# Performance work log

Hardware: AMD Instinct MI355X
Metric: run time of the kernel (lower is better)

The kernel has to match this reference:

```python
import jax, jax.numpy as jnp
import numpy as np

B, T, C = 4, 2048, 1024
H = 16
D = C // H  # head_dim = 64


def setup_inputs() -> dict:
    key = jax.random.key(0)
    ks = jax.random.split(key, 9)
    s = 1.0 / np.sqrt(C)
    return {
        "x": jax.random.normal(ks[0], (B, T, C), dtype=jnp.float32),
        "wq": jax.random.uniform(ks[1], (C, C), jnp.float32, -s, s),
        "bq": jax.random.uniform(ks[2], (C,), jnp.float32, -s, s),
        "wk": jax.random.uniform(ks[3], (C, C), jnp.float32, -s, s),
        "bk": jax.random.uniform(ks[4], (C,), jnp.float32, -s, s),
        "wv": jax.random.uniform(ks[5], (C, C), jnp.float32, -s, s),
        "bv": jax.random.uniform(ks[6], (C,), jnp.float32, -s, s),
        "wo": jax.random.uniform(ks[7], (C, C), jnp.float32, -s, s),
        "bo": jax.random.uniform(ks[8], (C,), jnp.float32, -s, s),
    }


def reference(x, wq, bq, wk, bk, wv, bv, wo, bo):
    # Linear layers (torch convention: y = x @ W.T + b)
    q = x @ wq.T + bq  # [B,T,C]
    k = x @ wk.T + bk
    v = x @ wv.T + bv
    # split heads -> [B,H,T,D]
    q = q.reshape(B, T, H, D).transpose(0, 2, 1, 3)
    k = k.reshape(B, T, H, D).transpose(0, 2, 1, 3)
    v = v.reshape(B, T, H, D).transpose(0, 2, 1, 3)
    scores = jnp.einsum('bhqd,bhkd->bhqk', q, k) / jnp.sqrt(jnp.float32(D))
    causal = jnp.tril(jnp.ones((T, T), dtype=bool))  # position i attends to j<=i
    scores = jnp.where(causal, scores, -jnp.inf)
    attn = jax.nn.softmax(scores, axis=-1)
    # dropout p=0.0 (eval / identity)
    out = jnp.einsum('bhqk,bhkd->bhqd', attn, v)  # [B,H,T,D]
    out = out.transpose(0, 2, 1, 3).reshape(B, T, C)
    return out @ wo.T + bo
```

## Files before the change

### kernel.cpp

```cpp
#include <hip/hip_runtime.h>
#include <stdint.h>

#define B_DIM 4
#define T_DIM 2048
#define C_DIM 1024
#define H_DIM 16
#define D_DIM 64
#define M_DIM (B_DIM * T_DIM)
#define QK_SCALE 0.18033688011112042f

typedef float f32x4 __attribute__((ext_vector_type(4)));
typedef float f32x16 __attribute__((ext_vector_type(16)));
typedef short bf16x8 __attribute__((ext_vector_type(8)));
typedef unsigned short u16;
typedef u16 u16x8 __attribute__((ext_vector_type(8)));

static __device__ __forceinline__ u16 f2b(float f) {
  uint32_t r;
  asm("v_cvt_pk_bf16_f32 %0, %1, %1" : "=v"(r) : "v"(f));
  return (u16)r;
}
static __device__ __forceinline__ uint32_t f2b2(float a, float b) {
  uint32_t r;
  asm("v_cvt_pk_bf16_f32 %0, %1, %2" : "=v"(r) : "v"(a), "v"(b));
  return r;
}

static __device__ __forceinline__ void gl_lds16(const u16* g, u16* l) {
  __builtin_amdgcn_global_load_lds(
      (const __attribute__((address_space(1))) void*)g,
      (__attribute__((address_space(3))) void*)l, 16, 0, 0);
}

__global__ void k_cvt(const float* __restrict__ src, u16* __restrict__ dst, int n4) {
  int i = blockIdx.x * blockDim.x + threadIdx.x;
  if (i < n4) {
    float4 v = ((const float4*)src)[i];
    uint2 o;
    o.x = f2b2(v.x, v.y);
    o.y = f2b2(v.z, v.w);
    ((uint2*)dst)[i] = o;
  }
}

__global__ void k_cvtw(const float* __restrict__ s0, const float* __restrict__ s1,
                       const float* __restrict__ s2, const float* __restrict__ s3,
                       u16* __restrict__ d0, u16* __restrict__ d1,
                       u16* __restrict__ d2, u16* __restrict__ d3) {
  int i = blockIdx.x * blockDim.x + threadIdx.x;
  int seg = i >> 18;
  int j = i & ((1 << 18) - 1);
  const float* s = seg == 0 ? s0 : seg == 1 ? s1 : seg == 2 ? s2 : s3;
  u16* d = seg == 0 ? d0 : seg == 1 ? d1 : seg == 2 ? d2 : d3;
  float4 v = ((const float4*)s)[j];
  uint2 o;
  o.x = f2b2(v.x, v.y);
  o.y = f2b2(v.z, v.w);
  ((uint2*)d)[j] = o;
}

__global__ __launch_bounds__(256) void k_gemm_qkv(
    const u16* __restrict__ A,
    const u16* __restrict__ w0, const u16* __restrict__ w1, const u16* __restrict__ w2,
    const float* __restrict__ b0, const float* __restrict__ b1, const float* __restrict__ b2,
    u16* __restrict__ Qo, u16* __restrict__ Ko, u16* __restrict__ Vo) {
  __shared__ u16 As[128 * 32];
  __shared__ u16 Bs[128 * 32];
  const int tid = threadIdx.x;
  const int l = tid & 63;
  const int w = tid >> 6;
  const int wr = w >> 1, wc = w & 1;
  const int seg = blockIdx.x >> 3;
  const int brow = blockIdx.y * 128, bcol = (blockIdx.x & 7) * 128;
  const int lrow = l & 15, lk = l >> 4;
  const int K = C_DIM;

  const u16* Bw = seg == 0 ? w0 : seg == 1 ? w1 : w2;
  const float* bias = seg == 0 ? b0 : seg == 1 ? b1 : b2;
  u16* Out = seg == 0 ? Qo : seg == 1 ? Ko : Vo;
  const float scale = seg == 0 ? QK_SCALE : 1.f;

  f32x4 acc[4][4];
  for (int m = 0; m < 4; ++m)
    for (int n = 0; n < 4; ++n)
      acc[m][n] = (f32x4){0.f, 0.f, 0.f, 0.f};

  for (int kt = 0; kt < K; kt += 32) {
    __syncthreads();
    {
      int slot = tid;
      int r0 = slot >> 2, c0 = slot & 3;
      gl_lds16(A + (size_t)(brow + r0) * K + kt + c0 * 8, As + slot * 8);
      gl_lds16(Bw + (size_t)(bcol + r0) * K + kt + c0 * 8, Bs + slot * 8);
      int slot2 = slot + 256;
      int r1 = slot2 >> 2, c1 = slot2 & 3;
      gl_lds16(A + (size_t)(brow + r1) * K + kt + c1 * 8, As + slot2 * 8);
      gl_lds16(Bw + (size_t)(bcol + r1) * K + kt + c1 * 8, Bs + slot2 * 8);
    }
    asm volatile("s_waitcnt vmcnt(0)" ::: "memory");
    __syncthreads();

    bf16x8 af[4], bfr[4];
#pragma unroll
    for (int m = 0; m < 4; ++m)
      af[m] = *(const bf16x8*)(As + (wr * 64 + m * 16 + lrow) * 32 + lk * 8);
#pragma unroll
    for (int n = 0; n < 4; ++n)
      bfr[n] = *(const bf16x8*)(Bs + (wc * 64 + n * 16 + lrow) * 32 + lk * 8);
#pragma unroll
    for (int m = 0; m < 4; ++m) {
#pragma unroll
      for (int n = 0; n < 4; ++n)
        acc[m][n] = __builtin_amdgcn_mfma_f32_16x16x32_bf16(af[m], bfr[n], acc[m][n], 0, 0, 0);
    }
  }

#pragma unroll
  for (int m = 0; m < 4; ++m) {
    int rg0 = brow + wr * 64 + m * 16 + lk * 4;
#pragma unroll
    for (int n = 0; n < 4; ++n) {
      int cg = bcol + wc * 64 + n * 16 + lrow;
      float bv = bias[cg];
#pragma unroll
      for (int i = 0; i < 4; ++i) {
        int rg = rg0 + i;
        float val = (acc[m][n][i] + bv) * scale;
        int bb = rg >> 11, tt = rg & (T_DIM - 1);
        int hh = cg >> 6, dd = cg & 63;
        Out[(((size_t)bb * H_DIM + hh) * T_DIM + tt) * D_DIM + dd] = f2b(val);
      }
    }
  }
}

__global__ __launch_bounds__(256) void k_gemm_proj(
    const u16* __restrict__ A, const u16* __restrict__ Bw,
    const float* __restrict__ bias, float* __restrict__ Cout) {
  __shared__ u16 As[128 * 32];
  __shared__ u16 Bs[128 * 32];
  const int tid = threadIdx.x;
  const int l = tid & 63;
  const int w = tid >> 6;
  const int wr = w >> 1, wc = w & 1;
  const int brow = blockIdx.y * 128, bcol = blockIdx.x * 128;
  const int lrow = l & 15, lk = l >> 4;
  const int K = C_DIM, N = C_DIM;

  f32x4 acc[4][4];
  for (int m = 0; m < 4; ++m)
    for (int n = 0; n < 4; ++n)
      acc[m][n] = (f32x4){0.f, 0.f, 0.f, 0.f};

  for (int kt = 0; kt < K; kt += 32) {
    __syncthreads();
    {
      int slot = tid;
      int r0 = slot >> 2, c0 = slot & 3;
      gl_lds16(A + (size_t)(brow + r0) * K + kt + c0 * 8, As + slot * 8);
      gl_lds16(Bw + (size_t)(bcol + r0) * K + kt + c0 * 8, Bs + slot * 8);
      int slot2 = slot + 256;
      int r1 = slot2 >> 2, c1 = slot2 & 3;
      gl_lds16(A + (size_t)(brow + r1) * K + kt + c1 * 8, As + slot2 * 8);
      gl_lds16(Bw + (size_t)(bcol + r1) * K + kt + c1 * 8, Bs + slot2 * 8);
    }
    asm volatile("s_waitcnt vmcnt(0)" ::: "memory");
    __syncthreads();

    bf16x8 af[4], bfr[4];
#pragma unroll
    for (int m = 0; m < 4; ++m)
      af[m] = *(const bf16x8*)(As + (wr * 64 + m * 16 + lrow) * 32 + lk * 8);
#pragma unroll
    for (int n = 0; n < 4; ++n)
      bfr[n] = *(const bf16x8*)(Bs + (wc * 64 + n * 16 + lrow) * 32 + lk * 8);
#pragma unroll
    for (int m = 0; m < 4; ++m) {
#pragma unroll
      for (int n = 0; n < 4; ++n)
        acc[m][n] = __builtin_amdgcn_mfma_f32_16x16x32_bf16(af[m], bfr[n], acc[m][n], 0, 0, 0);
    }
  }

#pragma unroll
  for (int m = 0; m < 4; ++m) {
    int rg0 = brow + wr * 64 + m * 16 + lk * 4;
#pragma unroll
    for (int n = 0; n < 4; ++n) {
      int cg = bcol + wc * 64 + n * 16 + lrow;
      float bv = bias[cg];
#pragma unroll
      for (int i = 0; i < 4; ++i)
        Cout[(size_t)(rg0 + i) * N + cg] = acc[m][n][i] + bv;
    }
  }
}

__global__ __launch_bounds__(256) void k_transpose(
    const u16* __restrict__ V, u16* __restrict__ Vt) {
  __shared__ u16 tile[64][65];
  const int tid = threadIdx.x;
  const int bh = blockIdx.y;
  const int t0 = blockIdx.x * 64;
  const size_t ibase = (size_t)bh * T_DIM * D_DIM + (size_t)t0 * D_DIM;
  const size_t obase = (size_t)bh * D_DIM * T_DIM + t0;

#pragma unroll
  for (int it = 0; it < 2; ++it) {
    int row = (tid >> 3) + it * 32;
    int blk = tid & 7;
    u16x8 v = *(const u16x8*)(V + ibase + (size_t)row * D_DIM + blk * 8);
#pragma unroll
    for (int j = 0; j < 8; ++j) tile[row][blk * 8 + j] = v[j];
  }
  __syncthreads();
#pragma unroll
  for (int it = 0; it < 2; ++it) {
    int d = (tid >> 3) + it * 32;
    int blk = tid & 7;
    u16x8 v;
#pragma unroll
    for (int j = 0; j < 8; ++j) v[j] = tile[blk * 8 + j][d];
    *(u16x8*)(Vt + obase + (size_t)d * T_DIM + blk * 8) = v;
  }
}

__global__ __launch_bounds__(256) void k_attn(
    const u16* __restrict__ Q, const u16* __restrict__ Kg,
    const u16* __restrict__ Vt, u16* __restrict__ O) {
  __shared__ u16 Ks[2][64 * 64];
  __shared__ u16 Vs[2][64 * 64];

  const int tid = threadIdx.x;
  const int l = tid & 63;
  const int w = tid >> 6;
  const int bh = blockIdx.x;
  const int qb = 15 - blockIdx.y;
  const int q0 = qb * 128;
  const int ql = l & 31;
  const int hi = l >> 5;
  const int r0 = q0 + w * 32;
  const int qg = r0 + ql;

  const size_t qkbase = (size_t)bh * T_DIM * D_DIM;
  const size_t vtbase = (size_t)bh * D_DIM * T_DIM;

  const int sr0 = tid >> 3, sc = tid & 7;
  const int sr1 = (tid + 256) >> 3;
  const int kcol0 = (sc ^ (sr0 & 7)) * 8;
  const int kcol1 = (sc ^ (sr1 & 7)) * 8;

#define STAGE(buf, kt)                                                                   \
  {                                                                                      \
    gl_lds16(Kg + qkbase + (size_t)((kt) * 64 + sr0) * D_DIM + kcol0, Ks[buf] + tid * 8);\
    gl_lds16(Vt + vtbase + (size_t)sr0 * T_DIM + (kt) * 64 + kcol0, Vs[buf] + tid * 8);  \
    gl_lds16(Kg + qkbase + (size_t)((kt) * 64 + sr1) * D_DIM + kcol1,                    \
             Ks[buf] + (tid + 256) * 8);                                                 \
    gl_lds16(Vt + vtbase + (size_t)sr1 * T_DIM + (kt) * 64 + kcol1,                      \
             Vs[buf] + (tid + 256) * 8);                                                 \
  }

  bf16x8 qf[4];
#pragma unroll
  for (int kk = 0; kk < 4; ++kk)
    qf[kk] = *(const bf16x8*)(Q + qkbase + (size_t)qg * D_DIM + kk * 16 + hi * 8);

  f32x16 oacc[2];
#pragma unroll
  for (int dt = 0; dt < 2; ++dt)
#pragma unroll
    for (int r = 0; r < 16; ++r) oacc[dt][r] = 0.f;
  float m_run = -1e30f, l_run = 0.f;

  const int tdiag = r0 >> 6;
  const int nkt = (q0 >> 6) + 2;

  STAGE(0, 0);

  for (int kt = 0; kt < nkt; ++kt) {
    const int cur = kt & 1;
    if (kt + 1 < nkt) {
      STAGE(cur ^ 1, kt + 1);
      asm volatile("s_waitcnt vmcnt(4)" ::: "memory");
    } else {
      asm volatile("s_waitcnt vmcnt(0)" ::: "memory");
    }
    __syncthreads();

    if (kt <= tdiag) {
      f32x16 s[2];
#pragma unroll
      for (int a = 0; a < 2; ++a)
#pragma unroll
        for (int r = 0; r < 16; ++r) s[a][r] = 0.f;

#pragma unroll
      for (int kk = 0; kk < 4; ++kk) {
#pragma unroll
        for (int a = 0; a < 2; ++a) {
          int row = a * 32 + ql;
          int blk = (kk * 2 + hi) ^ (row & 7);
          bf16x8 kf = *(const bf16x8*)(Ks[cur] + row * 64 + blk * 8);
          s[a] = __builtin_amdgcn_mfma_f32_32x32x16_bf16(kf, qf[kk], s[a], 0, 0, 0);
        }
      }

      if (kt == tdiag) {
#pragma unroll
        for (int a = 0; a < 2; ++a) {
#pragma unroll
          for (int r = 0; r < 16; ++r) {
            int kv = kt * 64 + a * 32 + (r & 3) + 8 * (r >> 2) + 4 * hi;
            if (kv > qg) s[a][r] = -1e30f;
          }
        }
      }

      float t[16];
#pragma unroll
      for (int r = 0; r < 16; ++r) t[r] = fmaxf(s[0][r], s[1][r]);
#pragma unroll
      for (int r = 0; r < 8; ++r) t[r] = fmaxf(t[r], t[r + 8]);
#pragma unroll
      for (int r = 0; r < 4; ++r) t[r] = fmaxf(t[r], t[r + 4]);
      float pm = fmaxf(fmaxf(t[0], t[1]), fmaxf(t[2], t[3]));
      pm = fmaxf(pm, __shfl_xor(pm, 32, 64));

      if (__any(pm > m_run + 8.f)) {
        float mn = fmaxf(m_run, pm);
        float sc = exp2f(m_run - mn);
        m_run = mn;
        l_run *= sc;
#pragma unroll
        for (int dt = 0; dt < 2; ++dt)
#pragma unroll
          for (int r = 0; r < 16; ++r) oacc[dt][r] *= sc;
      }

      float rs0 = 0.f, rs1 = 0.f, rs2 = 0.f, rs3 = 0.f;
#pragma unroll
      for (int a = 0; a < 2; ++a) {
#pragma unroll
        for (int r = 0; r < 16; ++r) {
          float p = exp2f(s[a][r] - m_run);
          s[a][r] = p;
          if ((r & 3) == 0) rs0 += p;
          else if ((r & 3) == 1) rs1 += p;
          else if ((r & 3) == 2) rs2 += p;
          else rs3 += p;
        }
      }
      float rs = (rs0 + rs1) + (rs2 + rs3);
      rs += __shfl_xor(rs, 32, 64);
      l_run += rs;

#pragma unroll
      for (int kk = 0; kk < 4; ++kk) {
        const int a = kk >> 1;
        const int base = (kk & 1) * 8;
        union { uint32_t wd[4]; bf16x8 v; } pf;
#pragma unroll
        for (int i = 0; i < 2; ++i) {
          uint32_t Aw = f2b2(s[a][base + 2 * i], s[a][base + 2 * i + 1]);
          uint32_t Bw = f2b2(s[a][base + 4 + 2 * i], s[a][base + 5 + 2 * i]);
          uint32_t As_ = (uint32_t)__shfl_xor((int)Aw, 32, 64);
          uint32_t Bs_ = (uint32_t)__shfl_xor((int)Bw, 32, 64);
          pf.wd[i] = hi ? Bs_ : Aw;
          pf.wd[2 + i] = hi ? Bw : As_;
        }
#pragma unroll
        for (int dt = 0; dt < 2; ++dt) {
          int row = dt * 32 + ql;
          int blk = (kk * 2 + hi) ^ (row & 7);
          bf16x8 vf = *(const bf16x8*)(Vs[cur] + row * 64 + blk * 8);
          oacc[dt] = __builtin_amdgcn_mfma_f32_32x32x16_bf16(vf, pf.v, oacc[dt], 0, 0, 0);
        }
      }
    }
    __syncthreads();
  }

  const int bb = bh >> 4, hh = bh & 15;
  const float inv = 1.f / l_run;
  u16* orow = O + ((size_t)bb * T_DIM + qg) * C_DIM + hh * D_DIM;
#pragma unroll
  for (int dt = 0; dt < 2; ++dt) {
#pragma unroll
    for (int g = 0; g < 4; ++g) {
      uint2 val;
      val.x = f2b2(oacc[dt][g * 4 + 0] * inv, oacc[dt][g * 4 + 1] * inv);
      val.y = f2b2(oacc[dt][g * 4 + 2] * inv, oacc[dt][g * 4 + 3] * inv);
      *(uint2*)(orow + dt * 32 + g * 8 + 4 * hi) = val;
    }
  }
}

extern "C" void kernel_launch(void* const* d_in, const int* in_sizes, int n_in,
                              void* d_out, int out_size, void* d_ws, size_t ws_size,
                              hipStream_t stream) {
  (void)in_sizes; (void)n_in; (void)out_size; (void)ws_size;
  const float* x  = (const float*)d_in[0];
  const float* wq = (const float*)d_in[1];
  const float* bq = (const float*)d_in[2];
  const float* wk = (const float*)d_in[3];
  const float* bk = (const float*)d_in[4];
  const float* wv = (const float*)d_in[5];
  const float* bv = (const float*)d_in[6];
  const float* wo = (const float*)d_in[7];
  const float* bo = (const float*)d_in[8];
  float* out = (float*)d_out;

  u16* xb  = (u16*)d_ws;
  u16* wqb = xb + (size_t)M_DIM * C_DIM;
  u16* wkb = wqb + (size_t)C_DIM * C_DIM;
  u16* wvb = wkb + (size_t)C_DIM * C_DIM;
  u16* wob = wvb + (size_t)C_DIM * C_DIM;
  u16* Qb  = wob + (size_t)C_DIM * C_DIM;
  u16* Kb  = Qb + (size_t)M_DIM * C_DIM;
  u16* Vb  = Kb + (size_t)M_DIM * C_DIM;
  u16* Vtb = Vb + (size_t)M_DIM * C_DIM;
  u16* Ob  = Vb;

  int n4x = M_DIM * C_DIM / 4;
  k_cvt<<<(n4x + 255) / 256, 256, 0, stream>>>(x, xb, n4x);
  k_cvtw<<<4096, 256, 0, stream>>>(wq, wk, wv, wo, wqb, wkb, wvb, wob);

  k_gemm_qkv<<<dim3(24, M_DIM / 128), 256, 0, stream>>>(
      xb, wqb, wkb, wvb, bq, bk, bv, Qb, Kb, Vb);

  k_transpose<<<dim3(T_DIM / 64, B_DIM * H_DIM), 256, 0, stream>>>(Vb, Vtb);
  k_attn<<<dim3(B_DIM * H_DIM, 16), 256, 0, stream>>>(Qb, Kb, Vtb, Ob);
  k_gemm_proj<<<dim3(C_DIM / 128, M_DIM / 128), 256, 0, stream>>>(Ob, wob, bo, out);
}
```

Measured before the change: 202.7 us.

## Rewrite QKV GEMM as 256x256 double-buffered pipelined tile with XCD swizzle

Replaces the QKV projection GEMM's 128x128 single-buffered tile with a 256x256 tile computed by 8 waves. Global-to-LDS loads for the next K step are double-buffered and interleaved with MFMA phases, using explicit barriers, waitcnt and setprio. A block-index swizzle groups tiles per XCD for better L2 reuse. This aims to hide load latency and raise arithmetic intensity, at the cost of more LDS (128KB per block), higher register pressure and more barriers.

```diff
diff --git a/kernel.cpp b/kernel.cpp
--- a/kernel.cpp
+++ b/kernel.cpp
@@ -59,79 +59,159 @@
   ((uint2*)d)[j] = o;
 }
 
-__global__ __launch_bounds__(256) void k_gemm_qkv(
+#define NT 16
+__global__ __launch_bounds__(512, 2) void k_gemm_qkv(
     const u16* __restrict__ A,
     const u16* __restrict__ w0, const u16* __restrict__ w1, const u16* __restrict__ w2,
     const float* __restrict__ b0, const float* __restrict__ b1, const float* __restrict__ b2,
     u16* __restrict__ Qo, u16* __restrict__ Ko, u16* __restrict__ Vo) {
-  __shared__ u16 As[128 * 32];
-  __shared__ u16 Bs[128 * 32];
+  __shared__ u16 LA[2][2][256 * 32];
+  __shared__ u16 LB[2][2][256 * 32];
   const int tid = threadIdx.x;
   const int l = tid & 63;
   const int w = tid >> 6;
-  const int wr = w >> 1, wc = w & 1;
-  const int seg = blockIdx.x >> 3;
-  const int brow = blockIdx.y * 128, bcol = (blockIdx.x & 7) * 128;
+  const int wm = w >> 2, wn = w & 3;
   const int lrow = l & 15, lk = l >> 4;
   const int K = C_DIM;
+
+  const int bid = blockIdx.x;
+  const int swz = (bid & 7) * 48 + (bid >> 3);
+  const int rowblk = swz / 12, colblk = swz % 12;
+  const int seg = colblk >> 2;
+  const int brow = rowblk * 256, bcol = (colblk & 3) * 256;
 
   const u16* Bw = seg == 0 ? w0 : seg == 1 ? w1 : w2;
   const float* bias = seg == 0 ? b0 : seg == 1 ? b1 : b2;
   u16* Out = seg == 0 ? Qo : seg == 1 ? Ko : Vo;
   const float scale = seg == 0 ? QK_SCALE : 1.f;
 
-  f32x4 acc[4][4];
-  for (int m = 0; m < 4; ++m)
-    for (int n = 0; n < 4; ++n)
-      acc[m][n] = (f32x4){0.f, 0.f, 0.f, 0.f};
-
-  for (int kt = 0; kt < K; kt += 32) {
-    __syncthreads();
-    {
-      int slot = tid;
-      int r0 = slot >> 2, c0 = slot & 3;
-      gl_lds16(A + (size_t)(brow + r0) * K + kt + c0 * 8, As + slot * 8);
-      gl_lds16(Bw + (size_t)(bcol + r0) * K + kt + c0 * 8, Bs + slot * 8);
-      int slot2 = slot + 256;
-      int r1 = slot2 >> 2, c1 = slot2 & 3;
-      gl_lds16(A + (size_t)(brow + r1) * K + kt + c1 * 8, As + slot2 * 8);
-      gl_lds16(Bw + (size_t)(bcol + r1) * K + kt + c1 * 8, Bs + slot2 * 8);
-    }
-    asm volatile("s_waitcnt vmcnt(0)" ::: "memory");
-    __syncthreads();
-
-    bf16x8 af[4], bfr[4];
-#pragma unroll
-    for (int m = 0; m < 4; ++m)
-      af[m] = *(const bf16x8*)(As + (wr * 64 + m * 16 + lrow) * 32 + lk * 8);
-#pragma unroll
-    for (int n = 0; n < 4; ++n)
-      bfr[n] = *(const bf16x8*)(Bs + (wc * 64 + n * 16 + lrow) * 32 + lk * 8);
-#pragma unroll
-    for (int m = 0; m < 4; ++m) {
-#pragma unroll
-      for (int n = 0; n < 4; ++n)
-        acc[m][n] = __builtin_amdgcn_mfma_f32_16x16x32_bf16(af[m], bfr[n], acc[m][n], 0, 0, 0);
-    }
-  }
-
-#pragma unroll
-  for (int m = 0; m < 4; ++m) {
-    int rg0 = brow + wr * 64 + m * 16 + lk * 4;
-#pragma unroll
-    for (int n = 0; n < 4; ++n) {
-      int cg = bcol + wc * 64 + n * 16 + lrow;
+  const int sr0 = tid >> 2, sc0 = (tid & 3) * 8;
+  const int sr1 = (tid + 512) >> 2;
+
+#define STA(db, kh, t)                                                              \
+  {                                                                                 \
+    gl_lds16(A + (size_t)(brow + sr0) * K + (t) * 64 + (kh) * 32 + sc0,             \
+             &LA[db][kh][sr0 * 32 + sc0]);                                          \
+    gl_lds16(A + (size_t)(brow + sr1) * K + (t) * 64 + (kh) * 32 + sc0,             \
+             &LA[db][kh][sr1 * 32 + sc0]);                                          \
+  }
+#define STB(db, kh, t)                                                              \
+  {                                                                                 \
+    gl_lds16(Bw + (size_t)(bcol + sr0) * K + (t) * 64 + (kh) * 32 + sc0,            \
+             &LB[db][kh][sr0 * 32 + sc0]);                                          \
+    gl_lds16(Bw + (size_t)(bcol + sr1) * K + (t) * 64 + (kh) * 32 + sc0,            \
+             &LB[db][kh][sr1 * 32 + sc0]);                                          \
+  }
+#define LDA_(f, kh, db) (*(const bf16x8*)(&LA[db][kh][(wm * 128 + (f) * 16 + lrow) * 32 + lk * 8]))
+#define LDB_(g, kh, db) (*(const bf16x8*)(&LB[db][kh][(wn * 64 + (g) * 16 + lrow) * 32 + lk * 8]))
+
+  f32x4 acc[8][4];
+#pragma unroll
+  for (int f = 0; f < 8; ++f)
+#pragma unroll
+    for (int g = 0; g < 4; ++g) acc[f][g] = (f32x4){0.f, 0.f, 0.f, 0.f};
+
+  STA(0, 0, 0); STB(0, 0, 0); STA(0, 1, 0); STB(0, 1, 0);
+  asm volatile("s_waitcnt vmcnt(0)" ::: "memory");
+  __syncthreads();
+
+  for (int t = 0; t < NT; ++t) {
+    const int db = t & 1, ndb = db ^ 1;
+    const bool pf = (t + 1 < NT);
+    bf16x8 afr[4], bfr[4];
+
+    if (pf) STA(ndb, 0, t + 1);
+#pragma unroll
+    for (int g = 0; g < 4; ++g) bfr[g] = LDB_(g, 0, db);
+#pragma unroll
+    for (int j = 0; j < 4; ++j) afr[j] = LDA_(j, 0, db);
+    __builtin_amdgcn_s_barrier();
+    asm volatile("s_waitcnt lgkmcnt(0)" ::: "memory");
+    __builtin_amdgcn_sched_barrier(0);
+    __builtin_amdgcn_s_setprio(1);
+#pragma unroll
+    for (int j = 0; j < 4; ++j)
+#pragma unroll
+      for (int g = 0; g < 4; ++g)
+        acc[j][g] = __builtin_amdgcn_mfma_f32_16x16x32_bf16(afr[j], bfr[g], acc[j][g], 0, 0, 0);
+    __builtin_amdgcn_s_setprio(0);
+    __builtin_amdgcn_s_barrier();
+
+    if (pf) STB(ndb, 0, t + 1);
+#pragma unroll
+    for (int j = 0; j < 4; ++j) afr[j] = LDA_(4 + j, 0, db);
+    __builtin_amdgcn_s_barrier();
+    asm volatile("s_waitcnt lgkmcnt(0)" ::: "memory");
+    __builtin_amdgcn_sched_barrier(0);
+    __builtin_amdgcn_s_setprio(1);
+#pragma unroll
+    for (int j = 0; j < 4; ++j)
+#pragma unroll
+      for (int g = 0; g < 4; ++g)
+        acc[4 + j][g] = __builtin_amdgcn_mfma_f32_16x16x32_bf16(afr[j], bfr[g], acc[4 + j][g], 0, 0, 0);
+    __builtin_amdgcn_s_setprio(0);
+    if (t == NT - 1) {
+      asm volatile("s_waitcnt vmcnt(0)" ::: "memory");
+    } else {
+      asm volatile("s_waitcnt vmcnt(4)" ::: "memory");
+    }
+    __builtin_amdgcn_s_barrier();
+
+    if (pf) STA(ndb, 1, t + 1);
+#pragma unroll
+    for (int g = 0; g < 4; ++g) bfr[g] = LDB_(g, 1, db);
+#pragma unroll
+    for (int j = 0; j < 4; ++j) afr[j] = LDA_(j, 1, db);
+    __builtin_amdgcn_s_barrier();
+    asm volatile("s_waitcnt lgkmcnt(0)" ::: "memory");
+    __builtin_amdgcn_sched_barrier(0);
+    __builtin_amdgcn_s_setprio(1);
+#pragma unroll
+    for (int j = 0; j < 4; ++j)
+#pragma unroll
+      for (int g = 0; g < 4; ++g)
+        acc[j][g] = __builtin_amdgcn_mfma_f32_16x16x32_bf16(afr[j], bfr[g], acc[j][g], 0, 0, 0);
+    __builtin_amdgcn_s_setprio(0);
+    __builtin_amdgcn_s_barrier();
+
+    if (pf) STB(ndb, 1, t + 1);
+#pragma unroll
+    for (int j = 0; j < 4; ++j) afr[j] = LDA_(4 + j, 1, db);
+    __builtin_amdgcn_s_barrier();
+    asm volatile("s_waitcnt lgkmcnt(0)" ::: "memory");
+    __builtin_amdgcn_sched_barrier(0);
+    __builtin_amdgcn_s_setprio(1);
+#pragma unroll
+    for (int j = 0; j < 4; ++j)
+#pragma unroll
+      for (int g = 0; g < 4; ++g)
+        acc[4 + j][g] = __builtin_amdgcn_mfma_f32_16x16x32_bf16(afr[j], bfr[g], acc[4 + j][g], 0, 0, 0);
+    __builtin_amdgcn_s_setprio(0);
+    asm volatile("s_waitcnt vmcnt(4)" ::: "memory");
+    __builtin_amdgcn_s_barrier();
+  }
+
+#pragma unroll
+  for (int f = 0; f < 8; ++f) {
+    int rg0 = brow + wm * 128 + f * 16 + lk * 4;
+#pragma unroll
+    for (int g = 0; g < 4; ++g) {
+      int cg = bcol + wn * 64 + g * 16 + lrow;
       float bv = bias[cg];
 #pragma unroll
       for (int i = 0; i < 4; ++i) {
         int rg = rg0 + i;
-        float val = (acc[m][n][i] + bv) * scale;
+        float val = (acc[f][g][i] + bv) * scale;
         int bb = rg >> 11, tt = rg & (T_DIM - 1);
         int hh = cg >> 6, dd = cg & 63;
         Out[(((size_t)bb * H_DIM + hh) * T_DIM + tt) * D_DIM + dd] = f2b(val);
       }
     }
   }
+#undef STA
+#undef STB
+#undef LDA_
+#undef LDB_
 }
 
 __global__ __launch_bounds__(256) void k_gemm_proj(
@@ -328,13 +408,13 @@
 
       if (__any(pm > m_run + 8.f)) {
         float mn = fmaxf(m_run, pm);
-        float sc = exp2f(m_run - mn);
+        float sc_ = exp2f(m_run - mn);
         m_run = mn;
-        l_run *= sc;
+        l_run *= sc_;
 #pragma unroll
         for (int dt = 0; dt < 2; ++dt)
 #pragma unroll
-          for (int r = 0; r < 16; ++r) oacc[dt][r] *= sc;
+          for (int r = 0; r < 16; ++r) oacc[dt][r] *= sc_;
       }
 
       float rs0 = 0.f, rs1 = 0.f, rs2 = 0.f, rs3 = 0.f;
@@ -425,7 +505,7 @@
   k_cvt<<<(n4x + 255) / 256, 256, 0, stream>>>(x, xb, n4x);
   k_cvtw<<<4096, 256, 0, stream>>>(wq, wk, wv, wo, wqb, wkb, wvb, wob);
 
-  k_gemm_qkv<<<dim3(24, M_DIM / 128), 256, 0, stream>>>(
+  k_gemm_qkv<<<384, 512, 0, stream>>>(
       xb, wqb, wkb, wvb, bq, bk, bv, Qb, Kb, Vb);
 
   k_transpose<<<dim3(T_DIM / 64, B_DIM * H_DIM), 256, 0, stream>>>(Vb, Vtb);
```

New measurement: 224.0 us. +10.5%, slower.
